# Kernel tuning notes

Hardware: AMD Instinct MI355X
Metric: run time of the kernel (lower is better)

The kernel has to match this reference:

```python
import jax, jax.numpy as jnp
import numpy as np

D = 120000   # sample_size
H1 = 600     # sample_size/200
H2 = 300     # sample_size/400
H3 = 200     # sample_size/600
DENSITY = 0.1  # sparselinear default connectivity
B = 512
EPS = 1e-5

_LAYER_SPECS = [(H1, D), (H1, H1), (H2, H1), (H3, H2), (H3, H3)]


def _make_idx(key, out_d, in_d, nnz):
    k1, k2 = jax.random.split(key)
    rows = jax.random.randint(k1, (nnz,), 0, out_d)
    cols = jax.random.randint(k2, (nnz,), 0, in_d)
    return jnp.stack([rows, cols]).astype(jnp.int32)


def setup_inputs() -> dict:
    key = jax.random.key(0)
    ks = jax.random.split(key, 32)
    inp = {"x": jax.random.normal(ks[0], (B, D), jnp.float32)}
    for i, (o, ii) in enumerate(_LAYER_SPECS, 1):
        nnz = int(DENSITY * o * ii)
        scale = 1.0 / np.sqrt(DENSITY * ii)  # kaiming-like fan-in scaling on nonzeros
        inp[f"idx{i}"] = _make_idx(ks[3 * i], o, ii, nnz)
        inp[f"val{i}"] = jax.random.normal(ks[3 * i + 1], (nnz,), jnp.float32) * scale
        inp[f"b{i}"] = jnp.zeros((o,), jnp.float32)
    for j, d in enumerate([H1, H2, H3], 1):
        inp[f"g{j}"] = jnp.ones((d,), jnp.float32)
        inp[f"be{j}"] = jnp.zeros((d,), jnp.float32)
    return inp


def _sp_linear(x, idx, vals, bias, out_d):
    # COO sparse linear: y = x @ W^T + b, W scattered from (row, col, val)
    in_d = x.shape[1]
    W = jnp.zeros((out_d, in_d), x.dtype).at[idx[0], idx[1]].add(vals)
    return x @ W.T + bias


def _bn(x, g, b):
    # BatchNorm1d, training mode: biased batch variance
    m = x.mean(axis=0)
    v = x.var(axis=0)
    return (x - m) * jax.lax.rsqrt(v + EPS) * g + b


def reference(x, idx1, val1, b1, idx2, val2, b2, idx3, val3, b3,
              idx4, val4, b4, idx5, val5, b5,
              g1, be1, g2, be2, g3, be3):
    h = jax.nn.silu(_bn(_sp_linear(x, idx1, val1, b1, H1), g1, be1))
    h = jax.nn.silu(_sp_linear(h, idx2, val2, b2, H1))
    h = jax.nn.silu(_bn(_sp_linear(h, idx3, val3, b3, H2), g2, be2))
    h = jax.nn.silu(_bn(_sp_linear(h, idx4, val4, b4, H3), g3, be3))
    return _sp_linear(h, idx5, val5, b5, H3)
```

## Files before the change

kernel.cpp:

```cpp
#include <hip/hip_runtime.h>

typedef unsigned short ushort_t;
typedef unsigned int uint_t;

typedef __bf16 bf16x8 __attribute__((ext_vector_type(8)));
typedef float  floatx4 __attribute__((ext_vector_type(4)));

#define AS3 __attribute__((address_space(3)))
#define AS1 __attribute__((address_space(1)))

#define BATCH 512
#define D_IN  120000
#define N1P   640
#define N2P   640
#define N3P   320
#define N4P   256
#define N5P   256

#define KSPLIT 30
#define KCHUNK 4000

#define HALF    60000
#define CHW     15000
#define NREG    1200
#define NB      256
#define RSTRIDE 6912

static constexpr long O_W1 = 0;
static constexpr long SZ_W1 = 640L * 120000 * 2;
static constexpr long O_W2 = O_W1 + SZ_W1;
static constexpr long SZ_W2 = 640L * 640 * 4;
static constexpr long O_W3 = O_W2 + SZ_W2;
static constexpr long SZ_W3 = 320L * 640 * 4;
static constexpr long O_W4 = O_W3 + SZ_W3;
static constexpr long SZ_W4 = 256L * 320 * 4;
static constexpr long O_W5 = O_W4 + SZ_W4;
static constexpr long SZ_W5 = 256L * 256 * 4;
static constexpr long O_Y1 = O_W5 + SZ_W5;
static constexpr long SZ_Y1 = 512L * 640 * 4;
static constexpr long ZERO_OFF = O_W2;
static constexpr long ZERO_BYTES = (O_Y1 + SZ_Y1) - O_W2;
static constexpr long O_SCR = O_Y1 + SZ_Y1;
static constexpr long O_CNT = O_SCR;
static constexpr long O_OFF = O_CNT + (long)NREG * NB * 4;
static constexpr long O_TOT = O_OFF + (long)NB * NREG * 4;
static constexpr long O_REC = O_TOT + 4800;
static constexpr long O_H1 = O_SCR;
static constexpr long O_H2 = O_H1 + 512L * 640 * 4;
static constexpr long O_Y3 = O_H2 + 512L * 640 * 4;
static constexpr long O_H3 = O_Y3 + 512L * 320 * 4;
static constexpr long O_Y4 = O_H3 + 512L * 320 * 4;
static constexpr long O_H4 = O_Y4 + 512L * 256 * 4;

__device__ __forceinline__ ushort_t f2bf(float f) {
    union { float f; uint_t u; } x;
    x.f = f;
    uint_t u = x.u;
    return (ushort_t)((u + 0x7FFFu + ((u >> 16) & 1u)) >> 16);
}
__device__ __forceinline__ uint_t cvt_pk_bf16(float lo, float hi) {
    uint_t r;
    asm("v_cvt_pk_bf16_f32 %0, %1, %2" : "=v"(r) : "v"(lo), "v"(hi));
    return r;
}
__device__ __forceinline__ float silu_f(float z) {
    return z / (1.f + expf(-z));
}
__device__ __forceinline__ void load16_lds(const void* g, void* l) {
    __builtin_amdgcn_global_load_lds((const AS1 char*)g, (AS3 char*)l, 16, 0, 0);
}

__global__ void zero_f4(float4* __restrict__ p, long n4) {
    long stride = (long)gridDim.x * blockDim.x;
    for (long i = (long)blockIdx.x * blockDim.x + threadIdx.x; i < n4; i += stride)
        p[i] = make_float4(0.f, 0.f, 0.f, 0.f);
}

__global__ __launch_bounds__(512) void hist1(const int* __restrict__ idx, int nnz, int chunk,
                                             int* __restrict__ counts ) {
    __shared__ uint_t h[NREG];
    const int b = blockIdx.x, t = threadIdx.x;
    for (int i = t; i < NREG; i += 512) h[i] = 0;
    __syncthreads();
    const int s = b * chunk;
    const int e = min(s + chunk, nnz);
    for (int i = s + t; i < e; i += 512) {
        int r = idx[i];
        int c = idx[nnz + i];
        atomicAdd(&h[r * 2 + (c >= HALF ? 1 : 0)], 1u);
    }
    __syncthreads();
    for (int i = t; i < NREG; i += 512) counts[(long)i * NB + b] = (int)h[i];
}

__global__ __launch_bounds__(NB) void scan1(const int* __restrict__ counts ,
                                            int* __restrict__ offs ,
                                            int* __restrict__ totals) {
    __shared__ int s[NB];
    const int reg = blockIdx.x, t = threadIdx.x;
    const int v = counts[(long)reg * NB + t];
    s[t] = v;
    __syncthreads();
    for (int o = 1; o < NB; o <<= 1) {
        int x = (t >= o) ? s[t - o] : 0;
        __syncthreads();
        s[t] += x;
        __syncthreads();
    }
    offs[(long)t * NREG + reg] = s[t] - v;
    if (t == NB - 1) totals[reg] = s[t];
}

__global__ __launch_bounds__(512) void scatter1(const int* __restrict__ idx,
                                                const float* __restrict__ vals,
                                                int nnz, int chunk,
                                                const int* __restrict__ offs ,
                                                int2* __restrict__ rec) {
    __shared__ int cur[NREG];
    const int b = blockIdx.x, t = threadIdx.x;
    const int* ob = offs + (long)b * NREG;
    for (int i = t; i < NREG; i += 512) cur[i] = i * RSTRIDE + ob[i];
    __syncthreads();
    const int s = b * chunk;
    const int e = min(s + chunk, nnz);
    for (int i = s + t; i < e; i += 512) {
        int r = idx[i];
        int c = idx[nnz + i];
        float v = vals[i];
        int h = (c >= HALF) ? 1 : 0;
        int reg = r * 2 + h;
        int slot = atomicAdd(&cur[reg], 1);
        if (slot < (reg + 1) * RSTRIDE)
            rec[slot] = make_int2(c - h * HALF, __float_as_int(v));
    }
}

__global__ __launch_bounds__(512) void build_w1(const int2* __restrict__ rec,
                                                const int* __restrict__ totals,
                                                ushort_t* __restrict__ W) {
    const int bid = blockIdx.x;
    const int r = bid >> 1, h = bid & 1;
    const int t = threadIdx.x;
    ushort_t* dstbase = W + (size_t)r * D_IN + h * HALF;

    if (r >= 600) {
        uint4 z = make_uint4(0, 0, 0, 0);
        for (int j = t * 8; j < HALF; j += 512 * 8) *(uint4*)(dstbase + j) = z;
        return;
    }

    __shared__ int2 lrec[RSTRIDE];
    __shared__ float acc[CHW];

    const int reg = r * 2 + h;
    const int n = min(totals[reg], RSTRIDE);
    const int2* src = rec + (long)reg * RSTRIDE;
    for (int i = t; i < n; i += 512) lrec[i] = src[i];
    __syncthreads();

#pragma unroll
    for (int ch = 0; ch < 4; ch++) {
        for (int j = t * 4; j < CHW; j += 512 * 4)
            *(float4*)&acc[j] = make_float4(0.f, 0.f, 0.f, 0.f);
        __syncthreads();
        const int base = ch * CHW;
        for (int i = t; i < n; i += 512) {
            int2 e = lrec[i];
            unsigned off = (unsigned)(e.x - base);
            if (off < (unsigned)CHW)
                atomicAdd(&acc[off], __int_as_float(e.y));
        }
        __syncthreads();
        ushort_t* dst = dstbase + base;
        for (int j = t * 8; j < CHW; j += 512 * 8) {
            union { ushort_t us[8]; uint4 v; } u;
#pragma unroll
            for (int k = 0; k < 8; k++) u.us[k] = f2bf(acc[j + k]);
            *(uint4*)(dst + j) = u.v;
        }
        __syncthreads();
    }
}

__global__ void scatter_all(const int* __restrict__ i2, const float* __restrict__ v2, int n2,
                            const int* __restrict__ i3, const float* __restrict__ v3, int n3,
                            const int* __restrict__ i4, const float* __restrict__ v4, int n4,
                            const int* __restrict__ i5, const float* __restrict__ v5, int n5,
                            float* __restrict__ W2, float* __restrict__ W3,
                            float* __restrict__ W4, float* __restrict__ W5) {
    int i = blockIdx.x * blockDim.x + threadIdx.x;
    if (i < n2) { atomicAdd(&W2[(size_t)i2[i] * 640 + i2[n2 + i]], v2[i]); return; }
    i -= n2;
    if (i < n3) { atomicAdd(&W3[(size_t)i3[i] * 640 + i3[n3 + i]], v3[i]); return; }
    i -= n3;
    if (i < n4) { atomicAdd(&W4[(size_t)i4[i] * 320 + i4[n4 + i]], v4[i]); return; }
    i -= n4;
    if (i < n5) { atomicAdd(&W5[(size_t)i5[i] * 256 + i5[n5 + i]], v5[i]); }
}

__global__ __launch_bounds__(256) void gemm1(const float* __restrict__ X,
                                             const ushort_t* __restrict__ W,
                                             float* __restrict__ Y) {
    __shared__ ushort_t sA[3][4096];
    __shared__ ushort_t sB[3][4096];

    const int b = blockIdx.x;
    const int wrk = (b & 7) * 75 + (b >> 3);
    const int ksIdx = wrk / 20;
    const int tile = wrk % 20;
    const int bm = tile / 5, bn = tile % 5;
    const int ks = ksIdx * KCHUNK;
    const int iters = KCHUNK / 32;

    const int t = threadIdx.x;
    const int lane = t & 63;
    const int w = t >> 6;
    const int wm = w >> 1, wn = w & 1;
    const int i16 = lane & 15;
    const int qk = lane >> 4;

    const int row0 = t >> 2;
    const int kq = (t & 3) ^ ((t >> 3) & 3);

    const float*    qa0 = X + (size_t)(bm * 128 + row0) * D_IN + ks + kq * 8;
    const float*    qa1 = qa0 + (size_t)64 * D_IN;
    const ushort_t* pb0 = W + (size_t)(bn * 128 + row0) * D_IN + ks + kq * 8;
    const ushort_t* pb1 = pb0 + (size_t)64 * D_IN;

    int aoff[4], boff[4];
#pragma unroll
    for (int mi = 0; mi < 4; mi++) {
        int row = wm * 64 + mi * 16 + i16;
        aoff[mi] = row * 64 + ((qk ^ ((row >> 1) & 3)) * 16);
    }
#pragma unroll
    for (int ni = 0; ni < 4; ni++) {
        int row = wn * 64 + ni * 16 + i16;
        boff[ni] = row * 64 + ((qk ^ ((row >> 1) & 3)) * 16);
    }
    const char* sAb = (const char*)sA;
    const char* sBb = (const char*)sB;

#define STAGEB(s) do {                                   \
        load16_lds(pb0, &sB[s][(w * 64) * 8]);           \
        load16_lds(pb1, &sB[s][(256 + w * 64) * 8]);     \
        pb0 += 32; pb1 += 32; } while (0)
#define LOADA(d0, d1, d2, d3) do {                       \
        d0 = *(const float4*)qa0;                        \
        d1 = *(const float4*)(qa0 + 4);                  \
        d2 = *(const float4*)qa1;                        \
        d3 = *(const float4*)(qa1 + 4);                  \
        qa0 += 32; qa1 += 32; } while (0)
#define WRITEA(s, d0, d1, d2, d3) do {                   \
        uint4 u0, u1;                                    \
        u0.x = cvt_pk_bf16(d0.x, d0.y); u0.y = cvt_pk_bf16(d0.z, d0.w); \
        u0.z = cvt_pk_bf16(d1.x, d1.y); u0.w = cvt_pk_bf16(d1.z, d1.w); \
        u1.x = cvt_pk_bf16(d2.x, d2.y); u1.y = cvt_pk_bf16(d2.z, d2.w); \
        u1.z = cvt_pk_bf16(d3.x, d3.y); u1.w = cvt_pk_bf16(d3.z, d3.w); \
        *(uint4*)&sA[s][t * 8] = u0;                     \
        *(uint4*)&sA[s][(t + 256) * 8] = u1; } while (0)

    floatx4 acc[4][4] = {};
    float4 p0, p1, p2, p3;
    float4 n0, n1, n2, n3;

    {
        float4 a0, a1, a2, a3;
        STAGEB(0);
        LOADA(a0, a1, a2, a3);
        STAGEB(1);
        LOADA(p0, p1, p2, p3);
        asm volatile("s_waitcnt vmcnt(6)" ::: "memory");
        WRITEA(0, a0, a1, a2, a3);
        asm volatile("s_waitcnt lgkmcnt(0)" ::: "memory");
    }
    __builtin_amdgcn_s_barrier();
    __builtin_amdgcn_sched_barrier(0);

    int cb = 0, wb = 1, nb = 2;
    for (int it = 0; it < iters; ++it) {
        if (it + 2 < iters) {
            STAGEB(nb);
            LOADA(n0, n1, n2, n3);
        }

        const int cbo = cb * 8192;
        bf16x8 af[4], bfr[4];
#pragma unroll
        for (int mi = 0; mi < 4; mi++)
            af[mi] = *(const bf16x8*)(sAb + cbo + aoff[mi]);
#pragma unroll
        for (int ni = 0; ni < 4; ni++)
            bfr[ni] = *(const bf16x8*)(sBb + cbo + boff[ni]);
#pragma unroll
        for (int mi = 0; mi < 4; mi++)
#pragma unroll
            for (int ni = 0; ni < 4; ni++)
                acc[mi][ni] = __builtin_amdgcn_mfma_f32_16x16x32_bf16(af[mi], bfr[ni], acc[mi][ni], 0, 0, 0);

        if (it + 1 < iters) {
            WRITEA(wb, p0, p1, p2, p3);
            p0 = n0; p1 = n1; p2 = n2; p3 = n3;
            asm volatile("s_waitcnt vmcnt(6)" ::: "memory");
            asm volatile("s_waitcnt lgkmcnt(0)" ::: "memory");
            __builtin_amdgcn_s_barrier();
            __builtin_amdgcn_sched_barrier(0);
        }
        int tmp = cb; cb = wb; wb = nb; nb = tmp;
    }
#undef STAGEB
#undef LOADA
#undef WRITEA

#pragma unroll
    for (int mi = 0; mi < 4; mi++) {
#pragma unroll
        for (int ni = 0; ni < 4; ni++) {
#pragma unroll
            for (int r = 0; r < 4; r++) {
                int row = bm * 128 + wm * 64 + mi * 16 + qk * 4 + r;
                int col = bn * 128 + wn * 64 + ni * 16 + i16;
                atomicAdd(&Y[(size_t)row * N1P + col], acc[mi][ni][r]);
            }
        }
    }
}

__global__ __launch_bounds__(512) void bn_silu(const float* __restrict__ Y, int ld, int realN,
                                               const float* __restrict__ g,
                                               const float* __restrict__ be,
                                               float* __restrict__ H) {
    const int t = threadIdx.x;
    const int sub = t >> 6;
    const int c = t & 63;
    const int col = blockIdx.x * 64 + c;

    float s = 0.f, ss = 0.f;
#pragma unroll 8
    for (int r = sub; r < BATCH; r += 8) {
        float v = Y[(size_t)r * ld + col];
        s += v;
        ss += v * v;
    }
    __shared__ float rs[8][64], rq[8][64], scs[64], shs[64];
    rs[sub][c] = s;
    rq[sub][c] = ss;
    __syncthreads();
    if (t < 64) {
        float S = 0.f, SS = 0.f;
#pragma unroll
        for (int k = 0; k < 8; k++) { S += rs[k][t]; SS += rq[k][t]; }
        float mean = S * (1.f / 512.f);
        float var  = SS * (1.f / 512.f) - mean * mean;
        int cc = blockIdx.x * 64 + t;
        float sc = 0.f, sh = 0.f;
        if (cc < realN) {
            sc = rsqrtf(var + 1e-5f) * g[cc];
            sh = be[cc] - mean * sc;
        }
        scs[t] = sc;
        shs[t] = sh;
    }
    __syncthreads();
    const float sc = scs[c], sh = shs[c];
#pragma unroll 8
    for (int r = sub; r < BATCH; r += 8) {
        float v = Y[(size_t)r * ld + col];
        H[(size_t)r * ld + col] = silu_f(v * sc + sh);
    }
}

template <int ACT, int GUARD>
__global__ __launch_bounds__(256) void small_gemm(const float* __restrict__ A, int lda,
                                                  const float* __restrict__ W, int ldw,
                                                  const float* __restrict__ bias, int biasN,
                                                  float* __restrict__ out, int ldo, int outN,
                                                  int K) {
    __shared__ float sA[64][20];
    __shared__ float sB[64][20];
    const int t = threadIdx.x;
    const int m0 = blockIdx.x * 64, n0 = blockIdx.y * 64;
    const int ty = t >> 4, tx = t & 15;
    const int lm = t >> 2, lq = t & 3;
    float acc[4][4] = {};

    for (int kt = 0; kt < K; kt += 16) {
        __syncthreads();
        float4 av = *(const float4*)&A[(size_t)(m0 + lm) * lda + kt + lq * 4];
        float4 wv = *(const float4*)&W[(size_t)(n0 + lm) * ldw + kt + lq * 4];
        sA[lm][lq * 4 + 0] = av.x; sA[lm][lq * 4 + 1] = av.y;
        sA[lm][lq * 4 + 2] = av.z; sA[lm][lq * 4 + 3] = av.w;
        sB[lm][lq * 4 + 0] = wv.x; sB[lm][lq * 4 + 1] = wv.y;
        sB[lm][lq * 4 + 2] = wv.z; sB[lm][lq * 4 + 3] = wv.w;
        __syncthreads();
#pragma unroll
        for (int kg = 0; kg < 4; kg++) {
            float4 a4[4], b4[4];
#pragma unroll
            for (int i = 0; i < 4; i++) a4[i] = *(const float4*)&sA[ty * 4 + i][kg * 4];
#pragma unroll
            for (int j = 0; j < 4; j++) b4[j] = *(const float4*)&sB[tx * 4 + j][kg * 4];
#pragma unroll
            for (int i = 0; i < 4; i++)
#pragma unroll
                for (int j = 0; j < 4; j++)
                    acc[i][j] += a4[i].x * b4[j].x + a4[i].y * b4[j].y +
                                 a4[i].z * b4[j].z + a4[i].w * b4[j].w;
        }
    }

#pragma unroll
    for (int i = 0; i < 4; i++) {
#pragma unroll
        for (int j = 0; j < 4; j++) {
            int row = m0 + ty * 4 + i;
            int col = n0 + tx * 4 + j;
            float v = acc[i][j];
            if (bias != nullptr && col < biasN) v += bias[col];
            if (ACT == 1) v = silu_f(v);
            if (GUARD) {
                if (col < outN) out[(size_t)row * ldo + col] = v;
            } else {
                out[(size_t)row * ldo + col] = v;
            }
        }
    }
}

extern "C" void kernel_launch(void* const* d_in, const int* in_sizes, int n_in,
                              void* d_out, int out_size, void* d_ws, size_t ws_size,
                              hipStream_t stream) {
    const float* x   = (const float*)d_in[0];
    const int* idx1 = (const int*)d_in[1];  const float* val1 = (const float*)d_in[2];
    const int* idx2 = (const int*)d_in[4];  const float* val2 = (const float*)d_in[5];
    const float* b2 = (const float*)d_in[6];
    const int* idx3 = (const int*)d_in[7];  const float* val3 = (const float*)d_in[8];
    const int* idx4 = (const int*)d_in[10]; const float* val4 = (const float*)d_in[11];
    const int* idx5 = (const int*)d_in[13]; const float* val5 = (const float*)d_in[14];
    const float* b5 = (const float*)d_in[15];
    const float* g1 = (const float*)d_in[16]; const float* be1 = (const float*)d_in[17];
    const float* g2 = (const float*)d_in[18]; const float* be2 = (const float*)d_in[19];
    const float* g3 = (const float*)d_in[20]; const float* be3 = (const float*)d_in[21];

    const int nnz1 = in_sizes[1] / 2;
    const int nnz2 = in_sizes[4] / 2;
    const int nnz3 = in_sizes[7] / 2;
    const int nnz4 = in_sizes[10] / 2;
    const int nnz5 = in_sizes[13] / 2;

    char* ws = (char*)d_ws;
    ushort_t* W1 = (ushort_t*)(ws + O_W1);
    float* W2 = (float*)(ws + O_W2);
    float* W3 = (float*)(ws + O_W3);
    float* W4 = (float*)(ws + O_W4);
    float* W5 = (float*)(ws + O_W5);
    float* y1 = (float*)(ws + O_Y1);
    int*   cnt = (int*)(ws + O_CNT);
    int*   off = (int*)(ws + O_OFF);
    int*   tot = (int*)(ws + O_TOT);
    int2*  rec = (int2*)(ws + O_REC);
    float* h1 = (float*)(ws + O_H1);
    float* h2 = (float*)(ws + O_H2);
    float* y3 = (float*)(ws + O_Y3);
    float* h3 = (float*)(ws + O_H3);
    float* y4 = (float*)(ws + O_Y4);
    float* h4 = (float*)(ws + O_H4);

    zero_f4<<<dim3((unsigned)(ZERO_BYTES / 16 / 256 + 1)), dim3(256), 0, stream>>>(
        (float4*)(ws + ZERO_OFF), ZERO_BYTES / 16);

    {
        const int chunk = (nnz1 + NB - 1) / NB;
        hist1<<<dim3(NB), dim3(512), 0, stream>>>(idx1, nnz1, chunk, cnt);
        scan1<<<dim3(NREG), dim3(NB), 0, stream>>>(cnt, off, tot);
        scatter1<<<dim3(NB), dim3(512), 0, stream>>>(idx1, val1, nnz1, chunk, off, rec);
        build_w1<<<dim3(640 * 2), dim3(512), 0, stream>>>(rec, tot, W1);
    }

    {
        int ntot = nnz2 + nnz3 + nnz4 + nnz5;
        scatter_all<<<dim3((ntot + 255) / 256), dim3(256), 0, stream>>>(
            idx2, val2, nnz2, idx3, val3, nnz3, idx4, val4, nnz4, idx5, val5, nnz5,
            W2, W3, W4, W5);
    }

    gemm1<<<dim3(8 * 75), dim3(256), 0, stream>>>(x, W1, y1);

    bn_silu<<<dim3(N1P / 64), dim3(512), 0, stream>>>(y1, N1P, 600, g1, be1, h1);

    small_gemm<1, 0><<<dim3(8, N2P / 64), dim3(256), 0, stream>>>(h1, N1P, W2, 640, b2, 600,
                                                                  h2, N2P, N2P, 640);
    small_gemm<0, 0><<<dim3(8, N3P / 64), dim3(256), 0, stream>>>(h2, N2P, W3, 640, nullptr, 0,
                                                                  y3, N3P, N3P, 640);
    bn_silu<<<dim3(N3P / 64), dim3(512), 0, stream>>>(y3, N3P, 300, g2, be2, h3);

    small_gemm<0, 0><<<dim3(8, N4P / 64), dim3(256), 0, stream>>>(h3, N3P, W4, 320, nullptr, 0,
                                                                  y4, N4P, N4P, 320);
    bn_silu<<<dim3(N4P / 64), dim3(512), 0, stream>>>(y4, N4P, 200, g3, be3, h4);

    small_gemm<0, 1><<<dim3(8, N5P / 64), dim3(256), 0, stream>>>(h4, N4P, W5, 256, b5, 200,
                                                                  (float*)d_out, 200, 200, 256);
    (void)n_in; (void)out_size; (void)ws_size;
}
```

Measured before the change: 1.033 ms.

## Retile gemm1 to 128x320 blocks with 512 threads and fewer K-splits

Changes the first GEMM's block tile from 128x128 to 128x320 (2 N-tiles instead of 5) with 512 threads per block. K is now split 25 ways at 4800 per chunk, which gives 200 blocks instead of 600. Each wave computes a 32x160 sub-tile, so one A fragment feeds more MFMAs and X is read from global fewer times. The cost is more LDS per block, more accumulator registers, fewer blocks to fill the GPU's compute units, and longer per-block K loops.

```diff
diff --git a/kernel.cpp b/kernel.cpp
--- a/kernel.cpp
+++ b/kernel.cpp
@@ -17,8 +17,8 @@
 #define N4P   256
 #define N5P   256
 
-#define KSPLIT 30
-#define KCHUNK 4000
+#define KSPLIT 25
+#define KCHUNK 4800
 
 #define HALF    60000
 #define CHW     15000
@@ -198,17 +198,17 @@
     if (i < n5) { atomicAdd(&W5[(size_t)i5[i] * 256 + i5[n5 + i]], v5[i]); }
 }
 
-__global__ __launch_bounds__(256) void gemm1(const float* __restrict__ X,
+__global__ __launch_bounds__(512) void gemm1(const float* __restrict__ X,
                                              const ushort_t* __restrict__ W,
                                              float* __restrict__ Y) {
     __shared__ ushort_t sA[3][4096];
-    __shared__ ushort_t sB[3][4096];
+    __shared__ ushort_t sB[3][12288];
 
     const int b = blockIdx.x;
-    const int wrk = (b & 7) * 75 + (b >> 3);
-    const int ksIdx = wrk / 20;
-    const int tile = wrk % 20;
-    const int bm = tile / 5, bn = tile % 5;
+    const int wrk = (b & 7) * 25 + (b >> 3);
+    const int ksIdx = wrk >> 3;
+    const int tile = wrk & 7;
+    const int bm = tile >> 1, bn = tile & 1;
     const int ks = ksIdx * KCHUNK;
     const int iters = KCHUNK / 32;
 
@@ -219,59 +219,52 @@
     const int i16 = lane & 15;
     const int qk = lane >> 4;
 
-    const int row0 = t >> 2;
-    const int kq = (t & 3) ^ ((t >> 3) & 3);
-
-    const float*    qa0 = X + (size_t)(bm * 128 + row0) * D_IN + ks + kq * 8;
-    const float*    qa1 = qa0 + (size_t)64 * D_IN;
-    const ushort_t* pb0 = W + (size_t)(bn * 128 + row0) * D_IN + ks + kq * 8;
-    const ushort_t* pb1 = pb0 + (size_t)64 * D_IN;
-
-    int aoff[4], boff[4];
-#pragma unroll
-    for (int mi = 0; mi < 4; mi++) {
-        int row = wm * 64 + mi * 16 + i16;
-        aoff[mi] = row * 64 + ((qk ^ ((row >> 1) & 3)) * 16);
-    }
-#pragma unroll
-    for (int ni = 0; ni < 4; ni++) {
-        int row = wn * 64 + ni * 16 + i16;
-        boff[ni] = row * 64 + ((qk ^ ((row >> 1) & 3)) * 16);
-    }
-    const char* sAb = (const char*)sA;
-    const char* sBb = (const char*)sB;
-
-#define STAGEB(s) do {                                   \
-        load16_lds(pb0, &sB[s][(w * 64) * 8]);           \
-        load16_lds(pb1, &sB[s][(256 + w * 64) * 8]);     \
-        pb0 += 32; pb1 += 32; } while (0)
-#define LOADA(d0, d1, d2, d3) do {                       \
-        d0 = *(const float4*)qa0;                        \
-        d1 = *(const float4*)(qa0 + 4);                  \
-        d2 = *(const float4*)qa1;                        \
-        d3 = *(const float4*)(qa1 + 4);                  \
-        qa0 += 32; qa1 += 32; } while (0)
-#define WRITEA(s, d0, d1, d2, d3) do {                   \
-        uint4 u0, u1;                                    \
-        u0.x = cvt_pk_bf16(d0.x, d0.y); u0.y = cvt_pk_bf16(d0.z, d0.w); \
-        u0.z = cvt_pk_bf16(d1.x, d1.y); u0.w = cvt_pk_bf16(d1.z, d1.w); \
-        u1.x = cvt_pk_bf16(d2.x, d2.y); u1.y = cvt_pk_bf16(d2.z, d2.w); \
-        u1.z = cvt_pk_bf16(d3.x, d3.y); u1.w = cvt_pk_bf16(d3.z, d3.w); \
-        *(uint4*)&sA[s][t * 8] = u0;                     \
-        *(uint4*)&sA[s][(t + 256) * 8] = u1; } while (0)
-
-    floatx4 acc[4][4] = {};
-    float4 p0, p1, p2, p3;
-    float4 n0, n1, n2, n3;
+    const int rowA = t >> 2;
+    const int kqA = (t & 3) ^ ((t >> 3) & 3);
+    const float* qa = X + (size_t)(bm * 128 + rowA) * D_IN + ks + kqA * 8;
+
+    const int cB1 = t + 512, cB2 = t + 1024;
+    const ushort_t* pb0 = W + (size_t)(bn * 320 + rowA) * D_IN + ks + kqA * 8;
+    const ushort_t* pb1 = W + (size_t)(bn * 320 + (cB1 >> 2)) * D_IN + ks
+                            + (((cB1 & 3) ^ ((cB1 >> 3) & 3))) * 8;
+    const ushort_t* pb2 = W + (size_t)(bn * 320 + (cB2 >> 2)) * D_IN + ks
+                            + (((cB2 & 3) ^ ((cB2 >> 3) & 3))) * 8;
+
+    int aoff[2], boff[10];
+#pragma unroll
+    for (int mi = 0; mi < 2; mi++) {
+        int row = wm * 32 + mi * 16 + i16;
+        aoff[mi] = row * 64 + ((qk ^ ((row >> 1) & 3)) << 4);
+    }
+#pragma unroll
+    for (int nf = 0; nf < 10; nf++) {
+        int row = wn * 160 + nf * 16 + i16;
+        boff[nf] = row * 64 + ((qk ^ ((row >> 1) & 3)) << 4);
+    }
+
+#define STAGEB(s) do {                                       \
+        load16_lds(pb0, &sB[s][(w * 64) * 8]);               \
+        load16_lds(pb1, &sB[s][(w * 64 + 512) * 8]);         \
+        load16_lds(pb2, &sB[s][(w * 64 + 1024) * 8]);        \
+        pb0 += 32; pb1 += 32; pb2 += 32; } while (0)
+#define WRITEA(s, d0, d1) do {                               \
+        uint4 u;                                             \
+        u.x = cvt_pk_bf16(d0.x, d0.y); u.y = cvt_pk_bf16(d0.z, d0.w); \
+        u.z = cvt_pk_bf16(d1.x, d1.y); u.w = cvt_pk_bf16(d1.z, d1.w); \
+        *(uint4*)&sA[s][t * 8] = u; } while (0)
+
+    floatx4 acc[2][10] = {};
+    float4 p0, p1;
+    float4 n0, n1;
 
     {
-        float4 a0, a1, a2, a3;
+        float4 a0, a1;
+        a0 = *(const float4*)qa; a1 = *(const float4*)(qa + 4); qa += 32;
         STAGEB(0);
-        LOADA(a0, a1, a2, a3);
+        p0 = *(const float4*)qa; p1 = *(const float4*)(qa + 4); qa += 32;
         STAGEB(1);
-        LOADA(p0, p1, p2, p3);
-        asm volatile("s_waitcnt vmcnt(6)" ::: "memory");
-        WRITEA(0, a0, a1, a2, a3);
+        WRITEA(0, a0, a1);
+        asm volatile("s_waitcnt vmcnt(5)" ::: "memory");
         asm volatile("s_waitcnt lgkmcnt(0)" ::: "memory");
     }
     __builtin_amdgcn_s_barrier();
@@ -280,28 +273,27 @@
     int cb = 0, wb = 1, nb = 2;
     for (int it = 0; it < iters; ++it) {
         if (it + 2 < iters) {
+            n0 = *(const float4*)qa; n1 = *(const float4*)(qa + 4); qa += 32;
             STAGEB(nb);
-            LOADA(n0, n1, n2, n3);
-        }
-
-        const int cbo = cb * 8192;
-        bf16x8 af[4], bfr[4];
-#pragma unroll
-        for (int mi = 0; mi < 4; mi++)
-            af[mi] = *(const bf16x8*)(sAb + cbo + aoff[mi]);
-#pragma unroll
-        for (int ni = 0; ni < 4; ni++)
-            bfr[ni] = *(const bf16x8*)(sBb + cbo + boff[ni]);
-#pragma unroll
-        for (int mi = 0; mi < 4; mi++)
-#pragma unroll
-            for (int ni = 0; ni < 4; ni++)
-                acc[mi][ni] = __builtin_amdgcn_mfma_f32_16x16x32_bf16(af[mi], bfr[ni], acc[mi][ni], 0, 0, 0);
+        }
+
+        bf16x8 af0 = *(const bf16x8*)((const char*)&sA[cb][0] + aoff[0]);
+        bf16x8 af1 = *(const bf16x8*)((const char*)&sA[cb][0] + aoff[1]);
+#pragma unroll
+        for (int nf = 0; nf < 10; nf++) {
+            bf16x8 bv = *(const bf16x8*)((const char*)&sB[cb][0] + boff[nf]);
+            acc[0][nf] = __builtin_amdgcn_mfma_f32_16x16x32_bf16(af0, bv, acc[0][nf], 0, 0, 0);
+            acc[1][nf] = __builtin_amdgcn_mfma_f32_16x16x32_bf16(af1, bv, acc[1][nf], 0, 0, 0);
+        }
 
         if (it + 1 < iters) {
-            WRITEA(wb, p0, p1, p2, p3);
-            p0 = n0; p1 = n1; p2 = n2; p3 = n3;
-            asm volatile("s_waitcnt vmcnt(6)" ::: "memory");
+            WRITEA(wb, p0, p1);
+            p0 = n0; p1 = n1;
+            if (it + 2 < iters) {
+                asm volatile("s_waitcnt vmcnt(5)" ::: "memory");
+            } else {
+                asm volatile("s_waitcnt vmcnt(0)" ::: "memory");
+            }
             asm volatile("s_waitcnt lgkmcnt(0)" ::: "memory");
             __builtin_amdgcn_s_barrier();
             __builtin_amdgcn_sched_barrier(0);
@@ -309,18 +301,17 @@
         int tmp = cb; cb = wb; wb = nb; nb = tmp;
     }
 #undef STAGEB
-#undef LOADA
 #undef WRITEA
 
 #pragma unroll
-    for (int mi = 0; mi < 4; mi++) {
-#pragma unroll
-        for (int ni = 0; ni < 4; ni++) {
+    for (int mi = 0; mi < 2; mi++) {
+#pragma unroll
+        for (int nf = 0; nf < 10; nf++) {
 #pragma unroll
             for (int r = 0; r < 4; r++) {
-                int row = bm * 128 + wm * 64 + mi * 16 + qk * 4 + r;
-                int col = bn * 128 + wn * 64 + ni * 16 + i16;
-                atomicAdd(&Y[(size_t)row * N1P + col], acc[mi][ni][r]);
+                int row = bm * 128 + wm * 32 + mi * 16 + qk * 4 + r;
+                int col = bn * 320 + wn * 160 + nf * 16 + i16;
+                atomicAdd(&Y[(size_t)row * N1P + col], acc[mi][nf][r]);
             }
         }
     }
@@ -484,7 +475,7 @@
             W2, W3, W4, W5);
     }
 
-    gemm1<<<dim3(8 * 75), dim3(256), 0, stream>>>(x, W1, y1);
+    gemm1<<<dim3(8 * KSPLIT), dim3(512), 0, stream>>>(x, W1, y1);
 
     bn_silu<<<dim3(N1P / 64), dim3(512), 0, stream>>>(y1, N1P, 600, g1, be1, h1);
 
```

New measurement: 1.045 ms. No clear change (+1.1%).
